# Kernel optimization log

Measured on AMD Instinct MI355X. Metric: run time of the kernel, lower is better.

The kernel has to match this reference:

```python
import jax, jax.numpy as jnp
import numpy as np

MAX_POS = 8192
SOFT_CAP = 5.0


def rms_norm(x, scale, eps=1e-6):
    # RMSBatchNorm approximated as RMS normalization over channels with learned scale
    return x * jax.lax.rsqrt(jnp.mean(x * x, axis=-1, keepdims=True) + eps) * scale


def layer_norm(x, scale, offset, eps=1e-5):
    mean = jnp.mean(x, axis=-1, keepdims=True)
    var = jnp.mean(jnp.square(x - mean), axis=-1, keepdims=True)
    return (x - mean) * jax.lax.rsqrt(var + eps) * scale + offset


def apply_rope(x, max_position=MAX_POS):
    # x: [B, S, H, C]
    B, S, H, C = x.shape
    positions = jnp.arange(S, dtype=x.dtype).reshape(1, S)
    num_freq = C // 2
    inv_freq = (1.0 / (jnp.arange(num_freq) + jnp.geomspace(1, max_position - num_freq + 1, num_freq))).astype(x.dtype)
    theta = jnp.einsum('bs,f->bsf', positions, inv_freq)
    theta = jnp.repeat(theta, 2, axis=-1)[..., None, :]  # [1, S, 1, C]
    x_rotated = jnp.stack([-x[..., 1::2], x[..., ::2]], axis=-1).reshape(x.shape)
    return x * jnp.cos(theta) + x_rotated * jnp.sin(theta)


def setup_inputs() -> dict:
    key = jax.random.key(0)
    ks = jax.random.split(key, 16)
    B, S, D = 2, 2048, 1536
    H, CQK, CV = 8, 128, 192
    inp = {
        'x': jax.random.normal(ks[0], (B, S, D), jnp.float32),
        'attention_bias': jax.random.normal(ks[1], (B, H, S, S), jnp.float32),
        'rms_in_scale': jnp.ones((D,), jnp.float32),
        'wq': jax.random.normal(ks[2], (D, H * CQK), jnp.float32) / np.sqrt(D),
        'wk': jax.random.normal(ks[3], (D, CQK), jnp.float32) / np.sqrt(D),
        'wv': jax.random.normal(ks[4], (D, CV), jnp.float32) / np.sqrt(D),
        'q_scale': jnp.ones((CQK,), jnp.float32),
        'q_offset': jnp.zeros((CQK,), jnp.float32),
        'k_scale': jnp.ones((CQK,), jnp.float32),
        'k_offset': jnp.zeros((CQK,), jnp.float32),
        'v_scale': jnp.ones((CV,), jnp.float32),
        'v_offset': jnp.zeros((CV,), jnp.float32),
        'wo': jax.random.normal(ks[5], (H * CV, D), jnp.float32) / np.sqrt(H * CV),
        'bo': jnp.zeros((D,), jnp.float32),
        'rms_out_scale': jnp.ones((D,), jnp.float32),
    }
    return inp


def reference(x, attention_bias, rms_in_scale, wq, wk, wv, q_scale, q_offset,
              k_scale, k_offset, v_scale, v_offset, wo, bo, rms_out_scale):
    B, S, D = x.shape
    H, CQK, CV = 8, 128, 192
    h = rms_norm(x, rms_in_scale)
    q = layer_norm((h @ wq).reshape(B, S, H, CQK), q_scale, q_offset)
    k = layer_norm((h @ wk).reshape(B, S, 1, CQK), k_scale, k_offset)
    v = layer_norm((h @ wv).reshape(B, S, 1, CV), v_scale, v_offset)
    q = apply_rope(q)
    k = apply_rope(k)
    # MQA logits: single shared K head
    logits = jnp.einsum('bshc,bSc->bhsS', q, k[:, :, 0], preferred_element_type=jnp.float32)
    logits = logits / np.sqrt(128.0)
    logits = (logits + attention_bias).astype(jnp.float32)
    logits = jnp.tanh(logits / SOFT_CAP) * SOFT_CAP
    weights = jax.nn.softmax(logits, axis=-1)
    y = jnp.einsum('bhsS,bSc->bshc', weights, v[:, :, 0]).astype(q.dtype)
    y = y.reshape(B, S, H * CV) @ wo + bo
    return rms_norm(y, rms_out_scale)
```

## Files before the change

kernel.cpp:

```cpp
#include <hip/hip_runtime.h>
#include <hip/hip_bf16.h>

typedef unsigned short u16;
typedef short bf16x8 __attribute__((ext_vector_type(8)));
typedef float f32x4 __attribute__((ext_vector_type(4)));

#define NB 2
#define NS 2048
#define ND 1536
#define NH 8
#define NCQK 128
#define NCV 192
#define NBS 4096
#define NPAD 1408

__device__ __forceinline__ float bf2f(u16 u) {
  unsigned v = ((unsigned)u) << 16;
  return __builtin_bit_cast(float, v);
}
__device__ __forceinline__ u16 f2bf(float f) {
  unsigned u = __builtin_bit_cast(unsigned, f);
  u += 0x7fffu + ((u >> 16) & 1u);
  return (u16)(u >> 16);
}
__device__ __forceinline__ void glds16(const u16* g, u16* l) {
  __builtin_amdgcn_global_load_lds(
      (const __attribute__((address_space(1))) void*)g,
      (__attribute__((address_space(3))) void*)l, 16, 0, 0);
}
__device__ __forceinline__ f32x4 mfma16(bf16x8 a, bf16x8 b, f32x4 c) {
  return __builtin_amdgcn_mfma_f32_16x16x32_bf16(a, b, c, 0, 0, 0);
}

__global__ void transpose_k(const float* __restrict__ in, u16* __restrict__ out,
                            int K, int N) {
  __shared__ float t[64][65];
  const int n0 = blockIdx.x * 64, k0 = blockIdx.y * 64;
  const int tid = threadIdx.x;
  const int rl = tid >> 4, cl = (tid & 15) * 4;
  for (int p = 0; p < 4; p++) {
    int k = rl + p * 16;
    float4 v = *(const float4*)(in + (size_t)(k0 + k) * N + n0 + cl);
    t[k][cl] = v.x; t[k][cl + 1] = v.y; t[k][cl + 2] = v.z; t[k][cl + 3] = v.w;
  }
  __syncthreads();
  const int rn = tid >> 3, ck = (tid & 7) * 8;
  for (int p = 0; p < 2; p++) {
    int n = rn + p * 32;
    u16 tmp[8];
    for (int j = 0; j < 8; j++) tmp[j] = f2bf(t[ck + j][n]);
    *(uint4*)(out + (size_t)(n0 + n) * K + k0 + ck) = *(uint4*)tmp;
  }
}

__global__ void rmsnorm_in_k(const float* __restrict__ x, const float* __restrict__ scale,
                             u16* __restrict__ h) {
  __shared__ float sbuf[4];
  const int row = blockIdx.x, tid = threadIdx.x;
  const float* xr = x + (size_t)row * ND;
  float v[6]; float ss = 0.f;
  for (int i = 0; i < 6; i++) { v[i] = xr[tid + i * 256]; ss += v[i] * v[i]; }
  for (int o = 32; o; o >>= 1) ss += __shfl_xor(ss, o);
  if ((tid & 63) == 0) sbuf[tid >> 6] = ss;
  __syncthreads();
  ss = sbuf[0] + sbuf[1] + sbuf[2] + sbuf[3];
  const float inv = rsqrtf(ss * (1.f / ND) + 1e-6f);
  u16* hr = h + (size_t)row * ND;
  for (int i = 0; i < 6; i++) {
    int c = tid + i * 256;
    hr[c] = f2bf(v[i] * inv * scale[c]);
  }
}

template <bool F32OUT>
__global__ __launch_bounds__(256, 2)
void gemm_nt(const u16* __restrict__ A, const u16* __restrict__ Bt,
             float* __restrict__ Cf, u16* __restrict__ Cb, int M, int N, int K) {
  __shared__ __align__(16) u16 As[2][64 * 128];
  __shared__ __align__(16) u16 Bs[2][64 * 128];
  const int tid = threadIdx.x;
  const int wave = tid >> 6, lane = tid & 63, quad = lane >> 4, l16 = lane & 15;
  const int m0 = blockIdx.y * 128, n0 = blockIdx.x * 128;
  const int mrb = (wave & 1) * 4, nrb = (wave >> 1) * 4;
  f32x4 acc[4][4] = {};

  auto stage = [&](int buf, int k0) {
#pragma unroll
    for (int i = 0; i < 4; i++) {
      int g = wave * 4 + i;
      int rb = g >> 1, kh = g & 1;
      int row = rb * 16 + l16, kc = kh * 4 + quad;
      glds16(A + (size_t)(m0 + row) * K + k0 + kc * 8, &As[buf][(rb * 8 + kh * 4) * 128]);
      glds16(Bt + (size_t)(n0 + row) * K + k0 + kc * 8, &Bs[buf][(rb * 8 + kh * 4) * 128]);
    }
  };

  const int nt = K >> 6;
  stage(0, 0);
  __syncthreads();
  for (int t = 0; t < nt; t++) {
    const int cur = t & 1;
    if (t + 1 < nt) stage(cur ^ 1, (t + 1) * 64);
#pragma unroll
    for (int kk = 0; kk < 2; kk++) {
      bf16x8 af[4], bfr[4];
#pragma unroll
      for (int f = 0; f < 4; f++)
        af[f] = *(const bf16x8*)&As[cur][(((mrb + f) * 8 + kk * 4 + quad) * 16 + l16) * 8];
#pragma unroll
      for (int f = 0; f < 4; f++)
        bfr[f] = *(const bf16x8*)&Bs[cur][(((nrb + f) * 8 + kk * 4 + quad) * 16 + l16) * 8];
#pragma unroll
      for (int mf = 0; mf < 4; mf++)
#pragma unroll
        for (int nf = 0; nf < 4; nf++)
          acc[mf][nf] = mfma16(af[mf], bfr[nf], acc[mf][nf]);
    }
    __syncthreads();
  }

  for (int mf = 0; mf < 4; mf++)
    for (int nf = 0; nf < 4; nf++)
      for (int r = 0; r < 4; r++) {
        int m = m0 + (wave & 1) * 64 + mf * 16 + quad * 4 + r;
        int n = n0 + (wave >> 1) * 64 + nf * 16 + l16;
        if (F32OUT) Cf[(size_t)m * N + n] = acc[mf][nf][r];
        else        Cb[(size_t)m * N + n] = f2bf(acc[mf][nf][r]);
      }
}

__global__ void ln_rope_k(const float* __restrict__ qkv,
                          const float* __restrict__ qs, const float* __restrict__ qo,
                          const float* __restrict__ ks, const float* __restrict__ ko,
                          const float* __restrict__ vs, const float* __restrict__ vo,
                          u16* __restrict__ Qg, u16* __restrict__ Kg, u16* __restrict__ Vg) {
  const int row = blockIdx.x;
  const int b = row >> 11, s = row & (NS - 1);
  const int wave = threadIdx.x >> 6, lane = threadIdx.x & 63;
  const float* base = qkv + (size_t)row * NPAD;
  const float gsp = __expf(logf(8129.f) * ((float)lane * (1.f / 63.f)));
  const float invf = 1.f / ((float)lane + gsp);
  float sn, cs;
  sincosf((float)s * invf, &sn, &cs);

  for (int hh = 0; hh < 2; hh++) {
    const int h = wave * 2 + hh;
    const float* p = base + h * NCQK;
    float x0 = p[lane * 2], x1 = p[lane * 2 + 1];
    float s1 = x0 + x1, s2 = x0 * x0 + x1 * x1;
    for (int o = 32; o; o >>= 1) { s1 += __shfl_xor(s1, o); s2 += __shfl_xor(s2, o); }
    float mean = s1 * (1.f / NCQK);
    float inv = rsqrtf(s2 * (1.f / NCQK) - mean * mean + 1e-5f);
    float y0 = (x0 - mean) * inv * qs[lane * 2] + qo[lane * 2];
    float y1 = (x1 - mean) * inv * qs[lane * 2 + 1] + qo[lane * 2 + 1];
    u16* dst = Qg + (size_t)row * (NH * NCQK) + h * NCQK + lane * 2;
    dst[0] = f2bf(y0 * cs - y1 * sn);
    dst[1] = f2bf(y1 * cs + y0 * sn);
  }
  if (wave == 0) {
    const float* p = base + NH * NCQK;
    float x0 = p[lane * 2], x1 = p[lane * 2 + 1];
    float s1 = x0 + x1, s2 = x0 * x0 + x1 * x1;
    for (int o = 32; o; o >>= 1) { s1 += __shfl_xor(s1, o); s2 += __shfl_xor(s2, o); }
    float mean = s1 * (1.f / NCQK);
    float inv = rsqrtf(s2 * (1.f / NCQK) - mean * mean + 1e-5f);
    float y0 = (x0 - mean) * inv * ks[lane * 2] + ko[lane * 2];
    float y1 = (x1 - mean) * inv * ks[lane * 2 + 1] + ko[lane * 2 + 1];
    u16* dst = Kg + (size_t)row * NCQK + lane * 2;
    dst[0] = f2bf(y0 * cs - y1 * sn);
    dst[1] = f2bf(y1 * cs + y0 * sn);
  }
  if (wave == 1) {
    const float* p = base + NH * NCQK + NCQK;
    float x[3]; float s1 = 0.f, s2 = 0.f;
    for (int i = 0; i < 3; i++) { x[i] = p[lane + i * 64]; s1 += x[i]; s2 += x[i] * x[i]; }
    for (int o = 32; o; o >>= 1) { s1 += __shfl_xor(s1, o); s2 += __shfl_xor(s2, o); }
    float mean = s1 * (1.f / NCV);
    float inv = rsqrtf(s2 * (1.f / NCV) - mean * mean + 1e-5f);
    for (int i = 0; i < 3; i++) {
      int c = lane + i * 64;
      float y = (x[i] - mean) * inv * vs[c] + vo[c];
      Vg[(size_t)(b * NCV + c) * NS + s] = f2bf(y);
    }
  }
}

__global__ __launch_bounds__(256, 2)
void attn_k(const u16* __restrict__ Qg, const u16* __restrict__ Kg,
            const u16* __restrict__ Vg, const float* __restrict__ bias,
            u16* __restrict__ Y) {
  __shared__ __align__(16) u16 smem[24576];
  __shared__ float lbuf[64];
  u16* Ks = smem;
  u16* Vs = smem + 8192;
  u16* Ps = smem + 20480;
  const int tid = threadIdx.x;
  const int wave = tid >> 6, lane = tid & 63, quad = lane >> 4, l16 = lane & 15;
  const int pair = wave >> 1, rw = wave & 1;
  const int s0 = blockIdx.x * 64;
  const int h = blockIdx.y, b = blockIdx.z;

  const float C1 = 0.0510069742f;
  const float C2 = 0.5770780163f;
  const float C3 = -14.4269504089f;
  const float C4 = 7.2134752044f;

  bf16x8 qa[2][4];
#pragma unroll
  for (int mf = 0; mf < 2; mf++) {
    const u16* qr = Qg + ((size_t)((b * NS + s0 + rw * 32 + mf * 16 + l16) * NH + h)) * NCQK;
#pragma unroll
    for (int kk = 0; kk < 4; kk++)
      qa[mf][kk] = *(const bf16x8*)(qr + (kk * 4 + quad) * 8);
  }

  const u16* Kbase = Kg + (size_t)(b * NS) * NCQK;
  const u16* Vbase = Vg + (size_t)(b * NCV) * NS;
  const float* brow = bias + ((size_t)(b * NH + h) * NS + s0 + rw * 32) * NS + pair * 32 + l16;

  auto stageK = [&](int key0) {
#pragma unroll
    for (int i = 0; i < 4; i++)
      glds16(Kbase + (size_t)(key0 + wave * 16 + l16) * NCQK + (i * 4 + quad) * 8,
             &Ks[(wave * 16 + i * 4) * 128]);
  };
  auto stageV = [&](int key0) {
#pragma unroll
    for (int i = 0; i < 6; i++) {
      int g = wave * 6 + i, cb = g >> 1, kh = g & 1;
      glds16(Vbase + (size_t)(cb * 16 + l16) * NS + key0 + (kh * 4 + quad) * 8,
             &Vs[(cb * 8 + kh * 4) * 128]);
    }
  };

  float breg[16];
  auto loadB = [&](int key0) {
#pragma unroll
    for (int mf = 0; mf < 2; mf++)
#pragma unroll
      for (int nb = 0; nb < 2; nb++)
#pragma unroll
        for (int r = 0; r < 4; r++)
          breg[(mf * 2 + nb) * 4 + r] = brow[(size_t)(mf * 16 + quad * 4 + r) * NS + key0 + nb * 16];
  };

  stageK(0);
  stageV(0);
  loadB(0);
  __syncthreads();

  f32x4 oacc[2][12] = {};
  float lsum[8] = {};

  const int pwb = wave * 1024;
  const int NT = NS / 64;

  for (int kt = 0; kt < NT; kt++) {
    f32x4 sacc[2][2] = {};
    __builtin_amdgcn_s_setprio(1);
#pragma unroll
    for (int kk = 0; kk < 4; kk++)
#pragma unroll
      for (int nb = 0; nb < 2; nb++) {
        bf16x8 kf = *(const bf16x8*)&Ks[(((pair * 2 + nb) * 16 + kk * 4 + quad) * 16 + l16) * 8];
        sacc[0][nb] = mfma16(qa[0][kk], kf, sacc[0][nb]);
        sacc[1][nb] = mfma16(qa[1][kk], kf, sacc[1][nb]);
      }
    __builtin_amdgcn_s_setprio(0);

#pragma unroll
    for (int mf = 0; mf < 2; mf++)
#pragma unroll
      for (int nb = 0; nb < 2; nb++) {
        const int xk = nb * 16 + l16;
#pragma unroll
        for (int r = 0; r < 4; r++) {
          float a = fmaf(sacc[mf][nb][r], C1, breg[(mf * 2 + nb) * 4 + r] * C2);
          float e2;
          asm("v_exp_f32 %0, %1" : "=v"(e2) : "v"(a));
          float u = __builtin_amdgcn_rcpf(e2 + 1.f);
          float a2 = fmaf(u, C3, C4);
          float p;
          asm("v_exp_f32 %0, %1" : "=v"(p) : "v"(a2));
          unsigned pk;
          asm("v_cvt_pk_bf16_f32 %0, %1, %2" : "=v"(pk) : "v"(p), "v"(p));
          lsum[mf * 4 + r] += __builtin_bit_cast(float, pk << 16);
          Ps[pwb + mf * 512 + (xk >> 3) * 128 + (quad * 4 + r) * 8 + (xk & 7)] = (u16)pk;
        }
      }

    __syncthreads();

    if (kt + 1 < NT) {
      stageK((kt + 1) * 64);
      loadB((kt + 1) * 64);
    }

    __builtin_amdgcn_s_setprio(1);
    bf16x8 pa0 = *(const bf16x8*)&Ps[pwb + quad * 128 + l16 * 8];
    bf16x8 pa1 = *(const bf16x8*)&Ps[pwb + 512 + quad * 128 + l16 * 8];
#pragma unroll
    for (int nb = 0; nb < 12; nb++) {
      bf16x8 vf = *(const bf16x8*)&Vs[((nb * 8 + pair * 4 + quad) * 16 + l16) * 8];
      oacc[0][nb] = mfma16(pa0, vf, oacc[0][nb]);
      oacc[1][nb] = mfma16(pa1, vf, oacc[1][nb]);
    }
    __builtin_amdgcn_s_setprio(0);

    __syncthreads();

    if (kt + 1 < NT) stageV((kt + 1) * 64);
  }

#pragma unroll
  for (int i = 0; i < 8; i++)
    for (int o = 1; o < 16; o <<= 1) lsum[i] += __shfl_xor(lsum[i], o);

  __syncthreads();
  float* smemF = (float*)smem;
  if (pair == 1) {
#pragma unroll
    for (int mf = 0; mf < 2; mf++) {
#pragma unroll
      for (int r = 0; r < 4; r++) {
        const int row = rw * 32 + mf * 16 + quad * 4 + r;
#pragma unroll
        for (int nb = 0; nb < 12; nb++)
          smemF[row * 192 + nb * 16 + l16] = oacc[mf][nb][r];
        if (l16 == 0) lbuf[row] = lsum[mf * 4 + r];
      }
    }
  }
  __syncthreads();
  if (pair == 0) {
#pragma unroll
    for (int mf = 0; mf < 2; mf++)
#pragma unroll
      for (int r = 0; r < 4; r++) {
        const int row = rw * 32 + mf * 16 + quad * 4 + r;
        const float inv = 1.f / (lsum[mf * 4 + r] + lbuf[row]);
        u16* yr = Y + (size_t)(b * NS + s0 + row) * ND + h * NCV;
#pragma unroll
        for (int nb = 0; nb < 12; nb++)
          yr[nb * 16 + l16] = f2bf((oacc[mf][nb][r] + smemF[row * 192 + nb * 16 + l16]) * inv);
      }
  }
}

__global__ void final_k(const u16* __restrict__ yo, const float* __restrict__ bo,
                        const float* __restrict__ scale, float* __restrict__ out) {
  __shared__ float sbuf[4];
  const int row = blockIdx.x, tid = threadIdx.x;
  const u16* yr = yo + (size_t)row * ND;
  float v[6]; float ss = 0.f;
  for (int i = 0; i < 6; i++) {
    int c = tid + i * 256;
    v[i] = bf2f(yr[c]) + bo[c];
    ss += v[i] * v[i];
  }
  for (int o = 32; o; o >>= 1) ss += __shfl_xor(ss, o);
  if ((tid & 63) == 0) sbuf[tid >> 6] = ss;
  __syncthreads();
  ss = sbuf[0] + sbuf[1] + sbuf[2] + sbuf[3];
  const float inv = rsqrtf(ss * (1.f / ND) + 1e-6f);
  float* orow = out + (size_t)row * ND;
  for (int i = 0; i < 6; i++) {
    int c = tid + i * 256;
    orow[c] = v[i] * inv * scale[c];
  }
}

extern "C" void kernel_launch(void* const* d_in, const int* in_sizes, int n_in,
                              void* d_out, int out_size, void* d_ws, size_t ws_size,
                              hipStream_t stream) {
  const float* x    = (const float*)d_in[0];
  const float* bias = (const float*)d_in[1];
  const float* rin  = (const float*)d_in[2];
  const float* wq   = (const float*)d_in[3];
  const float* wk   = (const float*)d_in[4];
  const float* wv   = (const float*)d_in[5];
  const float* qsc  = (const float*)d_in[6];
  const float* qof  = (const float*)d_in[7];
  const float* ksc  = (const float*)d_in[8];
  const float* kof  = (const float*)d_in[9];
  const float* vsc  = (const float*)d_in[10];
  const float* vof  = (const float*)d_in[11];
  const float* wo   = (const float*)d_in[12];
  const float* bo   = (const float*)d_in[13];
  const float* rout = (const float*)d_in[14];

  char* ws = (char*)d_ws;
  size_t off = 0;
  auto alloc = [&](size_t bytes) -> void* {
    void* p = ws + off;
    off += (bytes + 255) & ~(size_t)255;
    return p;
  };
  u16*   h    = (u16*)alloc((size_t)NBS * ND * 2);
  u16*   wtq  = (u16*)alloc((size_t)NPAD * ND * 2);
  u16*   wto  = (u16*)alloc((size_t)ND * ND * 2);
  float* qkv  = (float*)alloc((size_t)NBS * NPAD * 4);
  u16*   Qb   = (u16*)alloc((size_t)NBS * NH * NCQK * 2);
  u16*   Kb   = (u16*)alloc((size_t)NBS * NCQK * 2);
  u16*   Vtb  = (u16*)alloc((size_t)NB * NCV * NS * 2);
  u16*   Ybf  = (u16*)alloc((size_t)NBS * ND * 2);
  u16*   Yob  = (u16*)alloc((size_t)NBS * ND * 2);

  transpose_k<<<dim3(16, 24), 256, 0, stream>>>(wq, wtq, ND, 1024);
  transpose_k<<<dim3(2, 24), 256, 0, stream>>>(wk, wtq + (size_t)1024 * ND, ND, 128);
  transpose_k<<<dim3(3, 24), 256, 0, stream>>>(wv, wtq + (size_t)1152 * ND, ND, 192);
  transpose_k<<<dim3(24, 24), 256, 0, stream>>>(wo, wto, ND, ND);
  rmsnorm_in_k<<<NBS, 256, 0, stream>>>(x, rin, h);
  gemm_nt<true><<<dim3(NPAD / 128, NBS / 128), 256, 0, stream>>>(h, wtq, qkv, nullptr, NBS, NPAD, ND);
  ln_rope_k<<<NBS, 256, 0, stream>>>(qkv, qsc, qof, ksc, kof, vsc, vof, Qb, Kb, Vtb);
  attn_k<<<dim3(NS / 64, NH, NB), 256, 0, stream>>>(Qb, Kb, Vtb, bias, Ybf);
  gemm_nt<false><<<dim3(ND / 128, NBS / 128), 256, 0, stream>>>(Ybf, wto, nullptr, Yob, NBS, ND, ND);
  final_k<<<NBS, 256, 0, stream>>>(Yob, bo, rout, (float*)d_out);
}
```

Measured before the change: 583.6 us.

## Widen attention key tile to 128 and read V directly from global memory

The attention kernel now processes 128 keys per iteration instead of 64, halving the number of loop iterations and barriers. The K stage and the per-thread bias register buffer grow to match. V is no longer staged through shared memory; each wave loads its V fragments straight from global memory (through cache) for the PV MFMAs. This cuts LDS traffic and synchronisation but exposes global-load latency inside the MFMA loop and raises register pressure from the larger bias buffer.

```diff
diff --git a/kernel.cpp b/kernel.cpp
--- a/kernel.cpp
+++ b/kernel.cpp
@@ -192,8 +192,7 @@
   __shared__ __align__(16) u16 smem[24576];
   __shared__ float lbuf[64];
   u16* Ks = smem;
-  u16* Vs = smem + 8192;
-  u16* Ps = smem + 20480;
+  u16* Ps = smem + 16384;
   const int tid = threadIdx.x;
   const int wave = tid >> 6, lane = tid & 63, quad = lane >> 4, l16 = lane & 15;
   const int pair = wave >> 1, rw = wave & 1;
@@ -216,66 +215,58 @@
 
   const u16* Kbase = Kg + (size_t)(b * NS) * NCQK;
   const u16* Vbase = Vg + (size_t)(b * NCV) * NS;
-  const float* brow = bias + ((size_t)(b * NH + h) * NS + s0 + rw * 32) * NS + pair * 32 + l16;
+  const float* brow = bias + ((size_t)(b * NH + h) * NS + s0 + rw * 32) * NS + pair * 64 + l16;
 
   auto stageK = [&](int key0) {
 #pragma unroll
-    for (int i = 0; i < 4; i++)
-      glds16(Kbase + (size_t)(key0 + wave * 16 + l16) * NCQK + (i * 4 + quad) * 8,
-             &Ks[(wave * 16 + i * 4) * 128]);
+    for (int i = 0; i < 8; i++) {
+      int g = wave * 8 + i, kb = g >> 2, kh = g & 3;
+      glds16(Kbase + (size_t)(key0 + kb * 16 + l16) * NCQK + (kh * 4 + quad) * 8,
+             &Ks[(kb * 16 + kh * 4) * 128]);
+    }
   };
-  auto stageV = [&](int key0) {
-#pragma unroll
-    for (int i = 0; i < 6; i++) {
-      int g = wave * 6 + i, cb = g >> 1, kh = g & 1;
-      glds16(Vbase + (size_t)(cb * 16 + l16) * NS + key0 + (kh * 4 + quad) * 8,
-             &Vs[(cb * 8 + kh * 4) * 128]);
-    }
+
+  float breg[32];
+  auto loadB = [&](int key0) {
+#pragma unroll
+    for (int mf = 0; mf < 2; mf++)
+#pragma unroll
+      for (int nb = 0; nb < 4; nb++)
+#pragma unroll
+        for (int r = 0; r < 4; r++)
+          breg[(mf * 4 + nb) * 4 + r] =
+              brow[(size_t)(mf * 16 + quad * 4 + r) * NS + key0 + nb * 16];
   };
 
-  float breg[16];
-  auto loadB = [&](int key0) {
-#pragma unroll
-    for (int mf = 0; mf < 2; mf++)
-#pragma unroll
-      for (int nb = 0; nb < 2; nb++)
-#pragma unroll
-        for (int r = 0; r < 4; r++)
-          breg[(mf * 2 + nb) * 4 + r] = brow[(size_t)(mf * 16 + quad * 4 + r) * NS + key0 + nb * 16];
-  };
-
   stageK(0);
-  stageV(0);
   loadB(0);
   __syncthreads();
 
   f32x4 oacc[2][12] = {};
   float lsum[8] = {};
 
-  const int pwb = wave * 1024;
-  const int NT = NS / 64;
+  const int pwb = wave * 2048;
+  const int NT = NS / 128;
 
   for (int kt = 0; kt < NT; kt++) {
-    f32x4 sacc[2][2] = {};
-    __builtin_amdgcn_s_setprio(1);
-#pragma unroll
-    for (int kk = 0; kk < 4; kk++)
-#pragma unroll
-      for (int nb = 0; nb < 2; nb++) {
-        bf16x8 kf = *(const bf16x8*)&Ks[(((pair * 2 + nb) * 16 + kk * 4 + quad) * 16 + l16) * 8];
-        sacc[0][nb] = mfma16(qa[0][kk], kf, sacc[0][nb]);
-        sacc[1][nb] = mfma16(qa[1][kk], kf, sacc[1][nb]);
+#pragma unroll
+    for (int nb = 0; nb < 4; nb++) {
+      f32x4 sacc[2] = {};
+      __builtin_amdgcn_s_setprio(1);
+#pragma unroll
+      for (int kk = 0; kk < 4; kk++) {
+        bf16x8 kf = *(const bf16x8*)&Ks[(((pair * 4 + nb) * 16 + kk * 4 + quad) * 16 + l16) * 8];
+        sacc[0] = mfma16(qa[0][kk], kf, sacc[0]);
+        sacc[1] = mfma16(qa[1][kk], kf, sacc[1]);
       }
-    __builtin_amdgcn_s_setprio(0);
-
-#pragma unroll
-    for (int mf = 0; mf < 2; mf++)
-#pragma unroll
-      for (int nb = 0; nb < 2; nb++) {
-        const int xk = nb * 16 + l16;
+      __builtin_amdgcn_s_setprio(0);
+      const int ksub = nb >> 1;
+      const int xo = ((nb & 1) * 2 + (l16 >> 3)) * 128 + (l16 & 7);
+#pragma unroll
+      for (int mf = 0; mf < 2; mf++)
 #pragma unroll
         for (int r = 0; r < 4; r++) {
-          float a = fmaf(sacc[mf][nb][r], C1, breg[(mf * 2 + nb) * 4 + r] * C2);
+          float a = fmaf(sacc[mf][r], C1, breg[(mf * 4 + nb) * 4 + r] * C2);
           float e2;
           asm("v_exp_f32 %0, %1" : "=v"(e2) : "v"(a));
           float u = __builtin_amdgcn_rcpf(e2 + 1.f);
@@ -285,31 +276,33 @@
           unsigned pk;
           asm("v_cvt_pk_bf16_f32 %0, %1, %2" : "=v"(pk) : "v"(p), "v"(p));
           lsum[mf * 4 + r] += __builtin_bit_cast(float, pk << 16);
-          Ps[pwb + mf * 512 + (xk >> 3) * 128 + (quad * 4 + r) * 8 + (xk & 7)] = (u16)pk;
+          Ps[pwb + mf * 1024 + ksub * 512 + xo + (quad * 4 + r) * 8] = (u16)pk;
         }
+    }
+
+    __syncthreads();
+
+    if (kt + 1 < NT) {
+      stageK((kt + 1) * 128);
+      loadB((kt + 1) * 128);
+    }
+
+    __builtin_amdgcn_s_setprio(1);
+#pragma unroll
+    for (int ksub = 0; ksub < 2; ksub++) {
+      bf16x8 pa0 = *(const bf16x8*)&Ps[pwb + ksub * 512 + quad * 128 + l16 * 8];
+      bf16x8 pa1 = *(const bf16x8*)&Ps[pwb + 1024 + ksub * 512 + quad * 128 + l16 * 8];
+      const u16* vb = Vbase + kt * 128 + pair * 64 + ksub * 32 + quad * 8;
+#pragma unroll
+      for (int nb = 0; nb < 12; nb++) {
+        bf16x8 vf = *(const bf16x8*)(vb + (size_t)(nb * 16 + l16) * NS);
+        oacc[0][nb] = mfma16(pa0, vf, oacc[0][nb]);
+        oacc[1][nb] = mfma16(pa1, vf, oacc[1][nb]);
       }
+    }
+    __builtin_amdgcn_s_setprio(0);
 
     __syncthreads();
-
-    if (kt + 1 < NT) {
-      stageK((kt + 1) * 64);
-      loadB((kt + 1) * 64);
-    }
-
-    __builtin_amdgcn_s_setprio(1);
-    bf16x8 pa0 = *(const bf16x8*)&Ps[pwb + quad * 128 + l16 * 8];
-    bf16x8 pa1 = *(const bf16x8*)&Ps[pwb + 512 + quad * 128 + l16 * 8];
-#pragma unroll
-    for (int nb = 0; nb < 12; nb++) {
-      bf16x8 vf = *(const bf16x8*)&Vs[((nb * 8 + pair * 4 + quad) * 16 + l16) * 8];
-      oacc[0][nb] = mfma16(pa0, vf, oacc[0][nb]);
-      oacc[1][nb] = mfma16(pa1, vf, oacc[1][nb]);
-    }
-    __builtin_amdgcn_s_setprio(0);
-
-    __syncthreads();
-
-    if (kt + 1 < NT) stageV((kt + 1) * 64);
   }
 
 #pragma unroll
```

Measured after the change: 661.7 us. +13.4%, slower.
